# Performance work log

Measured on AMD Instinct MI355X. Metric: run time of the kernel, lower is better.

## Reference

```python
import jax, jax.numpy as jnp
import numpy as np

B, T, C, HS = 8, 2048, 1024, 64

def setup_inputs() -> dict:
    key = jax.random.key(0)
    kx, kq, kk, kv = jax.random.split(key, 4)
    x = jax.random.normal(kx, (B, T, C), dtype=jnp.float32)
    # Linear(C, HS, bias=False) weights, stored as [C, HS] so projection is x @ W
    Wq = jax.random.normal(kq, (C, HS), dtype=jnp.float32) * (C ** -0.5)
    Wk = jax.random.normal(kk, (C, HS), dtype=jnp.float32) * (C ** -0.5)
    Wv = jax.random.normal(kv, (C, HS), dtype=jnp.float32) * (C ** -0.5)
    return {"x": x, "Wq": Wq, "Wk": Wk, "Wv": Wv}

def reference(x, Wq, Wk, Wv):
    Bq, Tq, Cq = x.shape
    q = x @ Wq  # [B,T,HS]
    k = x @ Wk
    v = x @ Wv
    # NOTE: original scales by C**-0.5 with C = embedding_dim (not head_size)
    att = jnp.einsum('bqd,bkd->bqk', q, k) * (Cq ** -0.5)  # [B,T,T]
    causal = jnp.tril(jnp.ones((Tq, Tq), dtype=bool))
    att = jnp.where(causal, att, -jnp.inf)
    att = jax.nn.softmax(att, axis=-1)
    # dropout p=0.0 -> identity
    y = jnp.einsum('bqk,bkd->bqd', att, v)  # [B,T,HS]
    return y
```

## Files before the change

kernel.cpp:

```cpp
#include <hip/hip_runtime.h>
#include <hip/hip_bf16.h>
#include <math.h>

#define B_   8
#define T_   2048
#define C_   1024
#define HS_  64
#define MTOT (B_*T_)

typedef __attribute__((ext_vector_type(8))) short bf16x8;
typedef __attribute__((ext_vector_type(4))) float f32x4;
typedef __attribute__((ext_vector_type(8))) unsigned short u16x8;

static __device__ __forceinline__ unsigned short f2bf(float f) {
    __hip_bfloat16 h = __float2bfloat16(f);
    return *reinterpret_cast<unsigned short*>(&h);
}

__global__ __launch_bounds__(256) void cast_w_kernel(
    const float* __restrict__ Wq, const float* __restrict__ Wk,
    const float* __restrict__ Wv, unsigned short* __restrict__ Wt)
{
    const int tid = threadIdx.x;
    const int col = tid & 63;
    const int kc  = tid >> 6;
    const int mat = blockIdx.y;
    const int k0  = (blockIdx.x * 4 + kc) * 8;
    const float* __restrict__ W = (mat == 0) ? Wq : (mat == 1) ? Wk : Wv;
    const float s = (mat == 0) ? 0.03125f * 1.44269504f : 1.0f;

    u16x8 o;
#pragma unroll
    for (int i = 0; i < 8; ++i)
        o[i] = f2bf(W[(size_t)(k0 + i) * HS_ + col] * s);
    *(u16x8*)&Wt[(size_t)(mat * 64 + col) * C_ + k0] = o;
}

__global__ __launch_bounds__(512) void proj_gemm(
    const float* __restrict__ x, const unsigned short* __restrict__ Wt,
    unsigned short* __restrict__ qbf, unsigned short* __restrict__ kbf,
    unsigned short* __restrict__ vtbf)
{
    __shared__ unsigned short Als[2][64][72];
    __shared__ unsigned short Bls[2][192][72];

    const int tid  = threadIdx.x;
    const int lane = tid & 63;
    const int wv   = tid >> 6;
    const int wr   = wv & 1;
    const int cg   = wv >> 1;
    const int g    = lane >> 4;
    const int n15  = lane & 15;
    const int g4   = g * 4;
    const int m0   = blockIdx.x * 64;

    const int srow = tid >> 3;
    const int seg  = (tid & 7) * 8;
    const float* __restrict__ xrow = &x[(size_t)(m0 + srow) * C_ + seg];
    const unsigned short* __restrict__ wrow = &Wt[(size_t)srow * C_ + seg];

    f32x4 acc[2][3];
#pragma unroll
    for (int i = 0; i < 2; ++i)
#pragma unroll
        for (int j = 0; j < 3; ++j) acc[i][j] = (f32x4){0.f, 0.f, 0.f, 0.f};

    float4 a0[2], a1[2];
    int4   b0, b1, b2;

#define PROJ_LOAD_A(KC, S)                                              \
    do {                                                                \
        a0[S] = *(const float4*)&xrow[(KC) * 64 + 0];                   \
        a1[S] = *(const float4*)&xrow[(KC) * 64 + 4];                   \
    } while (0)

#define PROJ_LOAD_B(KC)                                                 \
    do {                                                                \
        b0 = *(const int4*)&wrow[(KC) * 64];                            \
        b1 = *(const int4*)&wrow[(size_t)64  * C_ + (KC) * 64];        \
        b2 = *(const int4*)&wrow[(size_t)128 * C_ + (KC) * 64];        \
    } while (0)

#define PROJ_WRITE_A(BUF, S)                                            \
    do {                                                                \
        u16x8 v0;                                                       \
        v0[0]=f2bf(a0[S].x); v0[1]=f2bf(a0[S].y);                       \
        v0[2]=f2bf(a0[S].z); v0[3]=f2bf(a0[S].w);                       \
        v0[4]=f2bf(a1[S].x); v0[5]=f2bf(a1[S].y);                       \
        v0[6]=f2bf(a1[S].z); v0[7]=f2bf(a1[S].w);                       \
        *(u16x8*)&Als[BUF][srow][seg] = v0;                             \
    } while (0)

#define PROJ_WRITE_B(BUF)                                               \
    do {                                                                \
        *(int4*)&Bls[BUF][srow][seg]        = b0;                       \
        *(int4*)&Bls[BUF][srow + 64][seg]   = b1;                       \
        *(int4*)&Bls[BUF][srow + 128][seg]  = b2;                       \
    } while (0)

    PROJ_LOAD_A(0, 0);
    PROJ_LOAD_B(0);
    PROJ_WRITE_A(0, 0);
    PROJ_WRITE_B(0);
    PROJ_LOAD_A(1, 1);
    __syncthreads();

    const int NK = C_ / 64;
    for (int kc = 0; kc < NK; ++kc) {
        const int cur = kc & 1;
        const int ka  = (kc + 2 < NK) ? kc + 2 : NK - 1;
        const int kb  = (kc + 1 < NK) ? kc + 1 : NK - 1;
        PROJ_LOAD_A(ka, kc & 1);
        PROJ_LOAD_B(kb);

#pragma unroll
        for (int kk = 0; kk < 2; ++kk) {
            bf16x8 fa0 = *(const bf16x8*)&Als[cur][wr * 32 + n15][kk * 32 + g * 8];
            bf16x8 fa1 = *(const bf16x8*)&Als[cur][wr * 32 + 16 + n15][kk * 32 + g * 8];
            bf16x8 fb0 = *(const bf16x8*)&Bls[cur][cg * 48 + n15][kk * 32 + g * 8];
            bf16x8 fb1 = *(const bf16x8*)&Bls[cur][cg * 48 + 16 + n15][kk * 32 + g * 8];
            bf16x8 fb2 = *(const bf16x8*)&Bls[cur][cg * 48 + 32 + n15][kk * 32 + g * 8];
            acc[0][0] = __builtin_amdgcn_mfma_f32_16x16x32_bf16(fa0, fb0, acc[0][0], 0, 0, 0);
            acc[0][1] = __builtin_amdgcn_mfma_f32_16x16x32_bf16(fa0, fb1, acc[0][1], 0, 0, 0);
            acc[0][2] = __builtin_amdgcn_mfma_f32_16x16x32_bf16(fa0, fb2, acc[0][2], 0, 0, 0);
            acc[1][0] = __builtin_amdgcn_mfma_f32_16x16x32_bf16(fa1, fb0, acc[1][0], 0, 0, 0);
            acc[1][1] = __builtin_amdgcn_mfma_f32_16x16x32_bf16(fa1, fb1, acc[1][1], 0, 0, 0);
            acc[1][2] = __builtin_amdgcn_mfma_f32_16x16x32_bf16(fa1, fb2, acc[1][2], 0, 0, 0);
        }

        if (kc + 1 < NK) {
            __syncthreads();
            PROJ_WRITE_A(cur ^ 1, (kc + 1) & 1);
            PROJ_WRITE_B(cur ^ 1);
            __syncthreads();
        }
    }
#undef PROJ_LOAD_A
#undef PROJ_LOAD_B
#undef PROJ_WRITE_A
#undef PROJ_WRITE_B

    __syncthreads();
    unsigned short* Cqk = &Als[0][0][0];
    unsigned short* Vtr = &Bls[0][0][0];

#pragma unroll
    for (int i = 0; i < 2; ++i)
#pragma unroll
        for (int j = 0; j < 3; ++j) {
            const int gcol = cg * 48 + j * 16 + n15;
            const int row0 = wr * 32 + i * 16 + g4;
            if (gcol < 128) {
#pragma unroll
                for (int r = 0; r < 4; ++r)
                    Cqk[(size_t)(row0 + r) * 136 + gcol] = f2bf(acc[i][j][r]);
            } else {
                ushort4 o;
                o.x = f2bf(acc[i][j][0]); o.y = f2bf(acc[i][j][1]);
                o.z = f2bf(acc[i][j][2]); o.w = f2bf(acc[i][j][3]);
                *(ushort4*)&Vtr[(size_t)(gcol - 128) * 72 + row0] = o;
            }
        }
    __syncthreads();

#pragma unroll
    for (int p = 0; p < 2; ++p) {
        const int flat = tid + p * 512;
        const int mat  = flat >> 9;
        const int r64  = (flat >> 3) & 63;
        const int sg   = (flat & 7) * 8;
        unsigned short* __restrict__ dst = mat ? kbf : qbf;
        *(int4*)&dst[(size_t)(m0 + r64) * HS_ + sg] =
            *(const int4*)&Cqk[(size_t)r64 * 136 + mat * 64 + sg];
    }
    {
        const int b  = m0 >> 11;
        const int t0 = m0 & 2047;
        const int hs = tid >> 3;
        *(int4*)&vtbf[((size_t)b * HS_ + hs) * T_ + t0 + seg] =
            *(const int4*)&Vtr[(size_t)hs * 72 + seg];
    }
}

__global__ __launch_bounds__(512) void attn_kernel(
    const unsigned short* __restrict__ qbf,
    const unsigned short* __restrict__ kbf,
    const unsigned short* __restrict__ vtbf,
    float* __restrict__ y)
{
    __shared__ unsigned short KVs[4][64][72];

    const int tid  = threadIdx.x;
    const int lane = tid & 63;
    const int wv   = tid >> 6;
    const int rg   = wv & 1;
    const int h    = (wv >> 1) & 1;
    const int tp   = wv >> 2;
    const int g    = lane >> 4;
    const int n15  = lane & 15;
    const int g4   = g * 4;
    const int b    = blockIdx.y;
    const size_t qkoff = (size_t)b * T_ * HS_;
    const size_t voff  = (size_t)b * HS_ * T_;

    const int sgrp = tid >> 8;
    const int st   = tid & 255;
    const int srow = st >> 3;
    const int soff = (st & 7) * 8;

    const unsigned short* __restrict__ kgb = &kbf[qkoff];
    const unsigned short* __restrict__ vgb = &vtbf[voff];

    const int qbi  = (blockIdx.y < 4) ? (int)blockIdx.x : 63 - (int)blockIdx.x;
    const int q0   = qbi * 32;
    const int qq0  = q0 + rg * 16;
    const int qrow = qq0 + n15;
    const int nkt  = (qbi >> 1) + 1;

    bf16x8 qf0 = *(const bf16x8*)&qbf[qkoff + (size_t)qrow * HS_ + g * 8];
    bf16x8 qf1 = *(const bf16x8*)&qbf[qkoff + (size_t)qrow * HS_ + g * 8 + 32];

    f32x4 o0 = {0.f,0.f,0.f,0.f}, o1 = o0, o2 = o0, o3 = o0;
    float mrow = -INFINITY, lrow = 0.f;

    int4 kr0, kr1, vr0, vr1;
    {
        int tix = (sgrp < nkt) ? sgrp : nkt - 1;
        kr0 = *(const int4*)&kgb[(size_t)(tix * 64 + srow) * HS_ + soff];
        kr1 = *(const int4*)&kgb[(size_t)(tix * 64 + srow + 32) * HS_ + soff];
        vr0 = *(const int4*)&vgb[(size_t)srow * T_ + tix * 64 + soff];
        vr1 = *(const int4*)&vgb[(size_t)(srow + 32) * T_ + tix * 64 + soff];
    }
    *(int4*)&KVs[sgrp][srow][soff]          = kr0;
    *(int4*)&KVs[sgrp][srow + 32][soff]     = kr1;
    *(int4*)&KVs[2 + sgrp][srow][soff]      = vr0;
    *(int4*)&KVs[2 + sgrp][srow + 32][soff] = vr1;
    __syncthreads();

    const int J = (nkt + 1) >> 1;
    for (int j = 0; j < J; ++j) {
        const int kt = 2 * j + tp;
        {
            int tix = 2 * j + sgrp + 2;
            if (tix > nkt - 1) tix = nkt - 1;
            kr0 = *(const int4*)&kgb[(size_t)(tix * 64 + srow) * HS_ + soff];
            kr1 = *(const int4*)&kgb[(size_t)(tix * 64 + srow + 32) * HS_ + soff];
            vr0 = *(const int4*)&vgb[(size_t)srow * T_ + tix * 64 + soff];
            vr1 = *(const int4*)&vgb[(size_t)(srow + 32) * T_ + tix * 64 + soff];
        }

        if (kt < nkt) {
            const int k0  = kt * 64;
            const int ks0 = h * 32;
            f32x4 st0 = {0.f,0.f,0.f,0.f}, st1 = st0;
            {
                bf16x8 ka;
                ka  = *(const bf16x8*)&KVs[tp][ks0 + n15][g * 8];
                st0 = __builtin_amdgcn_mfma_f32_16x16x32_bf16(ka, qf0, st0, 0, 0, 0);
                ka  = *(const bf16x8*)&KVs[tp][ks0 + n15][g * 8 + 32];
                st0 = __builtin_amdgcn_mfma_f32_16x16x32_bf16(ka, qf1, st0, 0, 0, 0);
                ka  = *(const bf16x8*)&KVs[tp][ks0 + 16 + n15][g * 8];
                st1 = __builtin_amdgcn_mfma_f32_16x16x32_bf16(ka, qf0, st1, 0, 0, 0);
                ka  = *(const bf16x8*)&KVs[tp][ks0 + 16 + n15][g * 8 + 32];
                st1 = __builtin_amdgcn_mfma_f32_16x16x32_bf16(ka, qf1, st1, 0, 0, 0);
            }

            const int kb = k0 + h * 32 + g4;
#pragma unroll
            for (int r = 0; r < 4; ++r) {
                if (kb + r      > qrow) st0[r] = -INFINITY;
                if (kb + 16 + r > qrow) st1[r] = -INFINITY;
            }

            float mloc = fmaxf(fmaxf(st0[0], st0[1]), fmaxf(st0[2], st0[3]));
            mloc = fmaxf(mloc, fmaxf(fmaxf(st1[0], st1[1]), fmaxf(st1[2], st1[3])));
            mloc = fmaxf(mloc, __shfl_xor(mloc, 16));
            mloc = fmaxf(mloc, __shfl_xor(mloc, 32));
            if (!__all(mloc <= mrow + 8.0f)) {
                float mnew  = fmaxf(mrow, mloc);
                float corr  = exp2f(mrow - fmaxf(mnew, -1e30f));
#pragma unroll
                for (int r = 0; r < 4; ++r) {
                    float cr = __shfl(corr, g4 + r);
                    o0[r] *= cr; o1[r] *= cr; o2[r] *= cr; o3[r] *= cr;
                }
                lrow *= corr;
                mrow  = mnew;
            }
            const float mb = fmaxf(mrow, -1e30f);
            float p[8];
            float psum = 0.f;
#pragma unroll
            for (int r = 0; r < 4; ++r) {
                p[r]     = exp2f(st0[r] - mb);
                p[4 + r] = exp2f(st1[r] - mb);
                psum += p[r] + p[4 + r];
            }
            psum += __shfl_xor(psum, 16);
            psum += __shfl_xor(psum, 32);
            lrow += psum;

            bf16x8 pa;
#pragma unroll
            for (int r = 0; r < 4; ++r) {
                pa[r]     = (short)f2bf(p[r]);
                pa[4 + r] = (short)f2bf(p[4 + r]);
            }

            const int kvo = h * 32;
            {
                ushort4 lo, hi; bf16x8 vb;
#define PV_STEP(NT, ONT)                                                        \
                lo = *(const ushort4*)&KVs[2 + tp][(NT)*16 + n15][kvo + g4];    \
                hi = *(const ushort4*)&KVs[2 + tp][(NT)*16 + n15][kvo + 16 + g4];\
                vb[0] = (short)lo.x; vb[1] = (short)lo.y;                       \
                vb[2] = (short)lo.z; vb[3] = (short)lo.w;                       \
                vb[4] = (short)hi.x; vb[5] = (short)hi.y;                       \
                vb[6] = (short)hi.z; vb[7] = (short)hi.w;                       \
                ONT = __builtin_amdgcn_mfma_f32_16x16x32_bf16(pa, vb, ONT, 0, 0, 0);
                PV_STEP(0, o0)
                PV_STEP(1, o1)
                PV_STEP(2, o2)
                PV_STEP(3, o3)
#undef PV_STEP
            }
        }

        if (j + 1 < J) {
            __syncthreads();
            *(int4*)&KVs[sgrp][srow][soff]          = kr0;
            *(int4*)&KVs[sgrp][srow + 32][soff]     = kr1;
            *(int4*)&KVs[2 + sgrp][srow][soff]      = vr0;
            *(int4*)&KVs[2 + sgrp][srow + 32][soff] = vr1;
            __syncthreads();
        }
    }

    __syncthreads();
    float* FS = (float*)&KVs[0][0][0];
    const int pid = (tp << 1) | h;
    if (pid != 0) {
        float* Ob = FS + (pid - 1) * 2176 + rg * 1088;
#pragma unroll
        for (int r = 0; r < 4; ++r) {
            Ob[(g4 + r) * 68 +  0 + n15] = o0[r];
            Ob[(g4 + r) * 68 + 16 + n15] = o1[r];
            Ob[(g4 + r) * 68 + 32 + n15] = o2[r];
            Ob[(g4 + r) * 68 + 48 + n15] = o3[r];
        }
        if (g == 0) {
            FS[6528 + (pid - 1) * 32 + rg * 16 + n15] = mrow;
            FS[6624 + (pid - 1) * 32 + rg * 16 + n15] = lrow;
        }
    }
    __syncthreads();
    if (pid == 0) {
        float m1 = FS[6528 +  0 + rg * 16 + n15];
        float m2 = FS[6528 + 32 + rg * 16 + n15];
        float m3 = FS[6528 + 64 + rg * 16 + n15];
        float l1 = FS[6624 +  0 + rg * 16 + n15];
        float l2 = FS[6624 + 32 + rg * 16 + n15];
        float l3 = FS[6624 + 64 + rg * 16 + n15];
        float mm = fmaxf(fmaxf(mrow, m1), fmaxf(m2, m3));
        float f0 = exp2f(mrow - mm);
        float f1 = exp2f(m1 - mm);
        float f2 = exp2f(m2 - mm);
        float f3 = exp2f(m3 - mm);
        float invl = 1.0f / (lrow * f0 + l1 * f1 + l2 * f2 + l3 * f3);
        const float* O1s = FS;
        const float* O2s = FS + 2176;
        const float* O3s = FS + 4352;
#pragma unroll
        for (int r = 0; r < 4; ++r) {
            float fr0 = __shfl(f0, g4 + r);
            float fr1 = __shfl(f1, g4 + r);
            float fr2 = __shfl(f2, g4 + r);
            float fr3 = __shfl(f3, g4 + r);
            float ir  = __shfl(invl, g4 + r);
            const int base = rg * 1088 + (g4 + r) * 68 + n15;
            float* yr = &y[((size_t)b * T_ + qq0 + g4 + r) * HS_];
            yr[ 0 + n15] = (o0[r] * fr0 + O1s[base]      * fr1 +
                            O2s[base]      * fr2 + O3s[base]      * fr3) * ir;
            yr[16 + n15] = (o1[r] * fr0 + O1s[base + 16] * fr1 +
                            O2s[base + 16] * fr2 + O3s[base + 16] * fr3) * ir;
            yr[32 + n15] = (o2[r] * fr0 + O1s[base + 32] * fr1 +
                            O2s[base + 32] * fr2 + O3s[base + 32] * fr3) * ir;
            yr[48 + n15] = (o3[r] * fr0 + O1s[base + 48] * fr1 +
                            O2s[base + 48] * fr2 + O3s[base + 48] * fr3) * ir;
        }
    }
}

extern "C" void kernel_launch(void* const* d_in, const int* in_sizes, int n_in,
                              void* d_out, int out_size, void* d_ws, size_t ws_size,
                              hipStream_t stream)
{
    const float* x  = (const float*)d_in[0];
    const float* Wq = (const float*)d_in[1];
    const float* Wk = (const float*)d_in[2];
    const float* Wv = (const float*)d_in[3];

    unsigned short* qbf  = (unsigned short*)d_ws;
    unsigned short* kbf  = qbf + (size_t)MTOT * HS_;
    unsigned short* vtbf = kbf + (size_t)MTOT * HS_;
    unsigned short* Wt   = vtbf + (size_t)MTOT * HS_;

    cast_w_kernel<<<dim3(32, 3), 256, 0, stream>>>(Wq, Wk, Wv, Wt);
    proj_gemm<<<256, 512, 0, stream>>>(x, Wt, qbf, kbf, vtbf);
    attn_kernel<<<dim3(64, B_), 512, 0, stream>>>(qbf, kbf, vtbf, (float*)d_out);
}
```

Measured before the change: 48.76 us.

## Pair causal query blocks per workgroup and triple-buffer K/V tiles with one barrier

Each attention workgroup now processes two query blocks, one short and one long (blockIdx.x and 63-blockIdx.x), so per-block causal work is balanced. Launched workgroups drop from 64 to 32 per batch. The K/V shared buffer becomes a three-slot ring with two register sets of prefetched tiles, which lets each iteration use one __syncthreads instead of two and writes the next tile before computing the current one. The cost is larger shared memory per block, possibly lower occupancy, and half as many blocks for the GPU to schedule.

```diff
diff --git a/kernel.cpp b/kernel.cpp
--- a/kernel.cpp
+++ b/kernel.cpp
@@ -188,7 +188,8 @@
     const unsigned short* __restrict__ vtbf,
     float* __restrict__ y)
 {
-    __shared__ unsigned short KVs[4][64][72];
+    __shared__ unsigned short Ksl[3][2][64][72];
+    __shared__ unsigned short Vsl[3][2][64][72];
 
     const int tid  = threadIdx.x;
     const int lane = tid & 63;
@@ -211,184 +212,217 @@
     const unsigned short* __restrict__ kgb = &kbf[qkoff];
     const unsigned short* __restrict__ vgb = &vtbf[voff];
 
-    const int qbi  = (blockIdx.y < 4) ? (int)blockIdx.x : 63 - (int)blockIdx.x;
-    const int q0   = qbi * 32;
-    const int qq0  = q0 + rg * 16;
-    const int qrow = qq0 + n15;
-    const int nkt  = (qbi >> 1) + 1;
-
-    bf16x8 qf0 = *(const bf16x8*)&qbf[qkoff + (size_t)qrow * HS_ + g * 8];
-    bf16x8 qf1 = *(const bf16x8*)&qbf[qkoff + (size_t)qrow * HS_ + g * 8 + 32];
-
-    f32x4 o0 = {0.f,0.f,0.f,0.f}, o1 = o0, o2 = o0, o3 = o0;
-    float mrow = -INFINITY, lrow = 0.f;
-
-    int4 kr0, kr1, vr0, vr1;
-    {
-        int tix = (sgrp < nkt) ? sgrp : nkt - 1;
-        kr0 = *(const int4*)&kgb[(size_t)(tix * 64 + srow) * HS_ + soff];
-        kr1 = *(const int4*)&kgb[(size_t)(tix * 64 + srow + 32) * HS_ + soff];
-        vr0 = *(const int4*)&vgb[(size_t)srow * T_ + tix * 64 + soff];
-        vr1 = *(const int4*)&vgb[(size_t)(srow + 32) * T_ + tix * 64 + soff];
+#define ATTN_LOADSET(K0, K1, V0, V1, TIX)                                   \
+    do {                                                                    \
+        K0 = *(const int4*)&kgb[(size_t)((TIX) * 64 + srow) * HS_ + soff];  \
+        K1 = *(const int4*)&kgb[(size_t)((TIX) * 64 + srow + 32) * HS_ + soff]; \
+        V0 = *(const int4*)&vgb[(size_t)srow * T_ + (TIX) * 64 + soff];     \
+        V1 = *(const int4*)&vgb[(size_t)(srow + 32) * T_ + (TIX) * 64 + soff]; \
+    } while (0)
+
+#define ATTN_WRITESET(K0, K1, V0, V1, SLOT)                                 \
+    do {                                                                    \
+        *(int4*)&Ksl[SLOT][sgrp][srow][soff]      = K0;                     \
+        *(int4*)&Ksl[SLOT][sgrp][srow + 32][soff] = K1;                     \
+        *(int4*)&Vsl[SLOT][sgrp][srow][soff]      = V0;                     \
+        *(int4*)&Vsl[SLOT][sgrp][srow + 32][soff] = V1;                     \
+    } while (0)
+
+#define ATTN_COMPUTE(SC)                                                    \
+    do {                                                                    \
+        const int k0  = kt * 64;                                            \
+        const int ks0 = h * 32;                                             \
+        f32x4 st0 = {0.f,0.f,0.f,0.f}, st1 = st0;                           \
+        {                                                                   \
+            bf16x8 ka;                                                      \
+            ka  = *(const bf16x8*)&Ksl[SC][tp][ks0 + n15][g * 8];           \
+            st0 = __builtin_amdgcn_mfma_f32_16x16x32_bf16(ka, qf0, st0, 0, 0, 0); \
+            ka  = *(const bf16x8*)&Ksl[SC][tp][ks0 + n15][g * 8 + 32];      \
+            st0 = __builtin_amdgcn_mfma_f32_16x16x32_bf16(ka, qf1, st0, 0, 0, 0); \
+            ka  = *(const bf16x8*)&Ksl[SC][tp][ks0 + 16 + n15][g * 8];      \
+            st1 = __builtin_amdgcn_mfma_f32_16x16x32_bf16(ka, qf0, st1, 0, 0, 0); \
+            ka  = *(const bf16x8*)&Ksl[SC][tp][ks0 + 16 + n15][g * 8 + 32]; \
+            st1 = __builtin_amdgcn_mfma_f32_16x16x32_bf16(ka, qf1, st1, 0, 0, 0); \
+        }                                                                   \
+        const int kb = k0 + h * 32 + g4;                                    \
+        _Pragma("unroll")                                                   \
+        for (int r = 0; r < 4; ++r) {                                       \
+            if (kb + r      > qrow) st0[r] = -INFINITY;                     \
+            if (kb + 16 + r > qrow) st1[r] = -INFINITY;                     \
+        }                                                                   \
+        float mloc = fmaxf(fmaxf(st0[0], st0[1]), fmaxf(st0[2], st0[3]));   \
+        mloc = fmaxf(mloc, fmaxf(fmaxf(st1[0], st1[1]), fmaxf(st1[2], st1[3]))); \
+        mloc = fmaxf(mloc, __shfl_xor(mloc, 16));                           \
+        mloc = fmaxf(mloc, __shfl_xor(mloc, 32));                           \
+        if (!__all(mloc <= mrow + 8.0f)) {                                  \
+            float mnew  = fmaxf(mrow, mloc);                                \
+            float corr  = exp2f(mrow - fmaxf(mnew, -1e30f));                \
+            _Pragma("unroll")                                               \
+            for (int r = 0; r < 4; ++r) {                                   \
+                float cr = __shfl(corr, g4 + r);                            \
+                o0[r] *= cr; o1[r] *= cr; o2[r] *= cr; o3[r] *= cr;         \
+            }                                                               \
+            lrow *= corr;                                                   \
+            mrow  = mnew;                                                   \
+        }                                                                   \
+        const float mb = fmaxf(mrow, -1e30f);                               \
+        float p[8];                                                         \
+        float psum = 0.f;                                                   \
+        _Pragma("unroll")                                                   \
+        for (int r = 0; r < 4; ++r) {                                       \
+            p[r]     = exp2f(st0[r] - mb);                                  \
+            p[4 + r] = exp2f(st1[r] - mb);                                  \
+            psum += p[r] + p[4 + r];                                        \
+        }                                                                   \
+        psum += __shfl_xor(psum, 16);                                       \
+        psum += __shfl_xor(psum, 32);                                       \
+        lrow += psum;                                                       \
+        bf16x8 pa;                                                          \
+        _Pragma("unroll")                                                   \
+        for (int r = 0; r < 4; ++r) {                                       \
+            pa[r]     = (short)f2bf(p[r]);                                  \
+            pa[4 + r] = (short)f2bf(p[4 + r]);                              \
+        }                                                                   \
+        const int kvo = h * 32;                                             \
+        {                                                                   \
+            ushort4 lo, hi; bf16x8 vb;                                      \
+            _Pragma("unroll")                                               \
+            for (int nt = 0; nt < 4; ++nt) {                                \
+                lo = *(const ushort4*)&Vsl[SC][tp][nt * 16 + n15][kvo + g4];      \
+                hi = *(const ushort4*)&Vsl[SC][tp][nt * 16 + n15][kvo + 16 + g4]; \
+                vb[0] = (short)lo.x; vb[1] = (short)lo.y;                   \
+                vb[2] = (short)lo.z; vb[3] = (short)lo.w;                   \
+                vb[4] = (short)hi.x; vb[5] = (short)hi.y;                   \
+                vb[6] = (short)hi.z; vb[7] = (short)hi.w;                   \
+                if (nt == 0) o0 = __builtin_amdgcn_mfma_f32_16x16x32_bf16(pa, vb, o0, 0, 0, 0); \
+                if (nt == 1) o1 = __builtin_amdgcn_mfma_f32_16x16x32_bf16(pa, vb, o1, 0, 0, 0); \
+                if (nt == 2) o2 = __builtin_amdgcn_mfma_f32_16x16x32_bf16(pa, vb, o2, 0, 0, 0); \
+                if (nt == 3) o3 = __builtin_amdgcn_mfma_f32_16x16x32_bf16(pa, vb, o3, 0, 0, 0); \
+            }                                                               \
+        }                                                                   \
+    } while (0)
+
+    for (int pass = 0; pass < 2; ++pass) {
+        const int qbi  = pass ? (63 - (int)blockIdx.x) : (int)blockIdx.x;
+        const int q0   = qbi * 32;
+        const int qq0  = q0 + rg * 16;
+        const int qrow = qq0 + n15;
+        const int nkt  = (qbi >> 1) + 1;
+        const int J    = (nkt + 1) >> 1;
+
+        bf16x8 qf0 = *(const bf16x8*)&qbf[qkoff + (size_t)qrow * HS_ + g * 8];
+        bf16x8 qf1 = *(const bf16x8*)&qbf[qkoff + (size_t)qrow * HS_ + g * 8 + 32];
+
+        f32x4 o0 = {0.f,0.f,0.f,0.f}, o1 = o0, o2 = o0, o3 = o0;
+        float mrow = -INFINITY, lrow = 0.f;
+
+        int4 kA0, kA1, vA0, vA1;
+        int4 kB0, kB1, vB0, vB1;
+
+        {
+            int tix = (sgrp < nkt) ? sgrp : nkt - 1;
+            ATTN_LOADSET(kA0, kA1, vA0, vA1, tix);
+        }
+        __syncthreads();
+        ATTN_WRITESET(kA0, kA1, vA0, vA1, 0);
+        {
+            int tix = 2 + sgrp; if (tix > nkt - 1) tix = nkt - 1;
+            ATTN_LOADSET(kB0, kB1, vB0, vB1, tix);
+        }
+        __syncthreads();
+
+        int j = 0;
+        while (true) {
+            {
+                if (j + 1 < J) {
+                    const int sN = (j + 1) % 3;
+                    ATTN_WRITESET(kB0, kB1, vB0, vB1, sN);
+                }
+                {
+                    int tix = 2 * (j + 2) + sgrp;
+                    if (tix > nkt - 1) tix = nkt - 1;
+                    ATTN_LOADSET(kA0, kA1, vA0, vA1, tix);
+                }
+                const int kt = 2 * j + tp;
+                const int sC = j % 3;
+                if (kt < nkt) ATTN_COMPUTE(sC);
+                __syncthreads();
+            }
+            if (++j >= J) break;
+            {
+                if (j + 1 < J) {
+                    const int sN = (j + 1) % 3;
+                    ATTN_WRITESET(kA0, kA1, vA0, vA1, sN);
+                }
+                {
+                    int tix = 2 * (j + 2) + sgrp;
+                    if (tix > nkt - 1) tix = nkt - 1;
+                    ATTN_LOADSET(kB0, kB1, vB0, vB1, tix);
+                }
+                const int kt = 2 * j + tp;
+                const int sC = j % 3;
+                if (kt < nkt) ATTN_COMPUTE(sC);
+                __syncthreads();
+            }
+            if (++j >= J) break;
+        }
+
+        float* FS = (float*)&Ksl[0][0][0][0];
+        const int pid = (tp << 1) | h;
+        if (pid != 0) {
+            float* Ob = FS + (pid - 1) * 2176 + rg * 1088;
+#pragma unroll
+            for (int r = 0; r < 4; ++r) {
+                Ob[(g4 + r) * 68 +  0 + n15] = o0[r];
+                Ob[(g4 + r) * 68 + 16 + n15] = o1[r];
+                Ob[(g4 + r) * 68 + 32 + n15] = o2[r];
+                Ob[(g4 + r) * 68 + 48 + n15] = o3[r];
+            }
+            if (g == 0) {
+                FS[6528 + (pid - 1) * 32 + rg * 16 + n15] = mrow;
+                FS[6624 + (pid - 1) * 32 + rg * 16 + n15] = lrow;
+            }
+        }
+        __syncthreads();
+        if (pid == 0) {
+            float m1 = FS[6528 +  0 + rg * 16 + n15];
+            float m2 = FS[6528 + 32 + rg * 16 + n15];
+            float m3 = FS[6528 + 64 + rg * 16 + n15];
+            float l1 = FS[6624 +  0 + rg * 16 + n15];
+            float l2 = FS[6624 + 32 + rg * 16 + n15];
+            float l3 = FS[6624 + 64 + rg * 16 + n15];
+            float mm = fmaxf(fmaxf(mrow, m1), fmaxf(m2, m3));
+            float f0 = exp2f(mrow - mm);
+            float f1 = exp2f(m1 - mm);
+            float f2 = exp2f(m2 - mm);
+            float f3 = exp2f(m3 - mm);
+            float invl = 1.0f / (lrow * f0 + l1 * f1 + l2 * f2 + l3 * f3);
+            const float* O1s = FS;
+            const float* O2s = FS + 2176;
+            const float* O3s = FS + 4352;
+#pragma unroll
+            for (int r = 0; r < 4; ++r) {
+                float fr0 = __shfl(f0, g4 + r);
+                float fr1 = __shfl(f1, g4 + r);
+                float fr2 = __shfl(f2, g4 + r);
+                float fr3 = __shfl(f3, g4 + r);
+                float ir  = __shfl(invl, g4 + r);
+                const int base = rg * 1088 + (g4 + r) * 68 + n15;
+                float* yr = &y[((size_t)b * T_ + qq0 + g4 + r) * HS_];
+                yr[ 0 + n15] = (o0[r] * fr0 + O1s[base]      * fr1 +
+                                O2s[base]      * fr2 + O3s[base]      * fr3) * ir;
+                yr[16 + n15] = (o1[r] * fr0 + O1s[base + 16] * fr1 +
+                                O2s[base + 16] * fr2 + O3s[base + 16] * fr3) * ir;
+                yr[32 + n15] = (o2[r] * fr0 + O1s[base + 32] * fr1 +
+                                O2s[base + 32] * fr2 + O3s[base + 32] * fr3) * ir;
+                yr[48 + n15] = (o3[r] * fr0 + O1s[base + 48] * fr1 +
+                                O2s[base + 48] * fr2 + O3s[base + 48] * fr3) * ir;
+            }
+        }
     }
-    *(int4*)&KVs[sgrp][srow][soff]          = kr0;
-    *(int4*)&KVs[sgrp][srow + 32][soff]     = kr1;
-    *(int4*)&KVs[2 + sgrp][srow][soff]      = vr0;
-    *(int4*)&KVs[2 + sgrp][srow + 32][soff] = vr1;
-    __syncthreads();
-
-    const int J = (nkt + 1) >> 1;
-    for (int j = 0; j < J; ++j) {
-        const int kt = 2 * j + tp;
-        {
-            int tix = 2 * j + sgrp + 2;
-            if (tix > nkt - 1) tix = nkt - 1;
-            kr0 = *(const int4*)&kgb[(size_t)(tix * 64 + srow) * HS_ + soff];
-            kr1 = *(const int4*)&kgb[(size_t)(tix * 64 + srow + 32) * HS_ + soff];
-            vr0 = *(const int4*)&vgb[(size_t)srow * T_ + tix * 64 + soff];
-            vr1 = *(const int4*)&vgb[(size_t)(srow + 32) * T_ + tix * 64 + soff];
-        }
-
-        if (kt < nkt) {
-            const int k0  = kt * 64;
-            const int ks0 = h * 32;
-            f32x4 st0 = {0.f,0.f,0.f,0.f}, st1 = st0;
-            {
-                bf16x8 ka;
-                ka  = *(const bf16x8*)&KVs[tp][ks0 + n15][g * 8];
-                st0 = __builtin_amdgcn_mfma_f32_16x16x32_bf16(ka, qf0, st0, 0, 0, 0);
-                ka  = *(const bf16x8*)&KVs[tp][ks0 + n15][g * 8 + 32];
-                st0 = __builtin_amdgcn_mfma_f32_16x16x32_bf16(ka, qf1, st0, 0, 0, 0);
-                ka  = *(const bf16x8*)&KVs[tp][ks0 + 16 + n15][g * 8];
-                st1 = __builtin_amdgcn_mfma_f32_16x16x32_bf16(ka, qf0, st1, 0, 0, 0);
-                ka  = *(const bf16x8*)&KVs[tp][ks0 + 16 + n15][g * 8 + 32];
-                st1 = __builtin_amdgcn_mfma_f32_16x16x32_bf16(ka, qf1, st1, 0, 0, 0);
-            }
-
-            const int kb = k0 + h * 32 + g4;
-#pragma unroll
-            for (int r = 0; r < 4; ++r) {
-                if (kb + r      > qrow) st0[r] = -INFINITY;
-                if (kb + 16 + r > qrow) st1[r] = -INFINITY;
-            }
-
-            float mloc = fmaxf(fmaxf(st0[0], st0[1]), fmaxf(st0[2], st0[3]));
-            mloc = fmaxf(mloc, fmaxf(fmaxf(st1[0], st1[1]), fmaxf(st1[2], st1[3])));
-            mloc = fmaxf(mloc, __shfl_xor(mloc, 16));
-            mloc = fmaxf(mloc, __shfl_xor(mloc, 32));
-            if (!__all(mloc <= mrow + 8.0f)) {
-                float mnew  = fmaxf(mrow, mloc);
-                float corr  = exp2f(mrow - fmaxf(mnew, -1e30f));
-#pragma unroll
-                for (int r = 0; r < 4; ++r) {
-                    float cr = __shfl(corr, g4 + r);
-                    o0[r] *= cr; o1[r] *= cr; o2[r] *= cr; o3[r] *= cr;
-                }
-                lrow *= corr;
-                mrow  = mnew;
-            }
-            const float mb = fmaxf(mrow, -1e30f);
-            float p[8];
-            float psum = 0.f;
-#pragma unroll
-            for (int r = 0; r < 4; ++r) {
-                p[r]     = exp2f(st0[r] - mb);
-                p[4 + r] = exp2f(st1[r] - mb);
-                psum += p[r] + p[4 + r];
-            }
-            psum += __shfl_xor(psum, 16);
-            psum += __shfl_xor(psum, 32);
-            lrow += psum;
-
-            bf16x8 pa;
-#pragma unroll
-            for (int r = 0; r < 4; ++r) {
-                pa[r]     = (short)f2bf(p[r]);
-                pa[4 + r] = (short)f2bf(p[4 + r]);
-            }
-
-            const int kvo = h * 32;
-            {
-                ushort4 lo, hi; bf16x8 vb;
-#define PV_STEP(NT, ONT)                                                        \
-                lo = *(const ushort4*)&KVs[2 + tp][(NT)*16 + n15][kvo + g4];    \
-                hi = *(const ushort4*)&KVs[2 + tp][(NT)*16 + n15][kvo + 16 + g4];\
-                vb[0] = (short)lo.x; vb[1] = (short)lo.y;                       \
-                vb[2] = (short)lo.z; vb[3] = (short)lo.w;                       \
-                vb[4] = (short)hi.x; vb[5] = (short)hi.y;                       \
-                vb[6] = (short)hi.z; vb[7] = (short)hi.w;                       \
-                ONT = __builtin_amdgcn_mfma_f32_16x16x32_bf16(pa, vb, ONT, 0, 0, 0);
-                PV_STEP(0, o0)
-                PV_STEP(1, o1)
-                PV_STEP(2, o2)
-                PV_STEP(3, o3)
-#undef PV_STEP
-            }
-        }
-
-        if (j + 1 < J) {
-            __syncthreads();
-            *(int4*)&KVs[sgrp][srow][soff]          = kr0;
-            *(int4*)&KVs[sgrp][srow + 32][soff]     = kr1;
-            *(int4*)&KVs[2 + sgrp][srow][soff]      = vr0;
-            *(int4*)&KVs[2 + sgrp][srow + 32][soff] = vr1;
-            __syncthreads();
-        }
-    }
-
-    __syncthreads();
-    float* FS = (float*)&KVs[0][0][0];
-    const int pid = (tp << 1) | h;
-    if (pid != 0) {
-        float* Ob = FS + (pid - 1) * 2176 + rg * 1088;
-#pragma unroll
-        for (int r = 0; r < 4; ++r) {
-            Ob[(g4 + r) * 68 +  0 + n15] = o0[r];
-            Ob[(g4 + r) * 68 + 16 + n15] = o1[r];
-            Ob[(g4 + r) * 68 + 32 + n15] = o2[r];
-            Ob[(g4 + r) * 68 + 48 + n15] = o3[r];
-        }
-        if (g == 0) {
-            FS[6528 + (pid - 1) * 32 + rg * 16 + n15] = mrow;
-            FS[6624 + (pid - 1) * 32 + rg * 16 + n15] = lrow;
-        }
-    }
-    __syncthreads();
-    if (pid == 0) {
-        float m1 = FS[6528 +  0 + rg * 16 + n15];
-        float m2 = FS[6528 + 32 + rg * 16 + n15];
-        float m3 = FS[6528 + 64 + rg * 16 + n15];
-        float l1 = FS[6624 +  0 + rg * 16 + n15];
-        float l2 = FS[6624 + 32 + rg * 16 + n15];
-        float l3 = FS[6624 + 64 + rg * 16 + n15];
-        float mm = fmaxf(fmaxf(mrow, m1), fmaxf(m2, m3));
-        float f0 = exp2f(mrow - mm);
-        float f1 = exp2f(m1 - mm);
-        float f2 = exp2f(m2 - mm);
-        float f3 = exp2f(m3 - mm);
-        float invl = 1.0f / (lrow * f0 + l1 * f1 + l2 * f2 + l3 * f3);
-        const float* O1s = FS;
-        const float* O2s = FS + 2176;
-        const float* O3s = FS + 4352;
-#pragma unroll
-        for (int r = 0; r < 4; ++r) {
-            float fr0 = __shfl(f0, g4 + r);
-            float fr1 = __shfl(f1, g4 + r);
-            float fr2 = __shfl(f2, g4 + r);
-            float fr3 = __shfl(f3, g4 + r);
-            float ir  = __shfl(invl, g4 + r);
-            const int base = rg * 1088 + (g4 + r) * 68 + n15;
-            float* yr = &y[((size_t)b * T_ + qq0 + g4 + r) * HS_];
-            yr[ 0 + n15] = (o0[r] * fr0 + O1s[base]      * fr1 +
-                            O2s[base]      * fr2 + O3s[base]      * fr3) * ir;
-            yr[16 + n15] = (o1[r] * fr0 + O1s[base + 16] * fr1 +
-                            O2s[base + 16] * fr2 + O3s[base + 16] * fr3) * ir;
-            yr[32 + n15] = (o2[r] * fr0 + O1s[base + 32] * fr1 +
-                            O2s[base + 32] * fr2 + O3s[base + 32] * fr3) * ir;
-            yr[48 + n15] = (o3[r] * fr0 + O1s[base + 48] * fr1 +
-                            O2s[base + 48] * fr2 + O3s[base + 48] * fr3) * ir;
-        }
-    }
+#undef ATTN_LOADSET
+#undef ATTN_WRITESET
+#undef ATTN_COMPUTE
 }
 
 extern "C" void kernel_launch(void* const* d_in, const int* in_sizes, int n_in,
@@ -407,5 +441,5 @@
 
     cast_w_kernel<<<dim3(32, 3), 256, 0, stream>>>(Wq, Wk, Wv, Wt);
     proj_gemm<<<256, 512, 0, stream>>>(x, Wt, qbf, kbf, vtbf);
-    attn_kernel<<<dim3(64, B_), 512, 0, stream>>>(qbf, kbf, vtbf, (float*)d_out);
+    attn_kernel<<<dim3(32, B_), 512, 0, stream>>>(qbf, kbf, vtbf, (float*)d_out);
 }
```

Result: no change. 49.58 us (+1.7%).

## Process two 32-row query sets per K/V tile and pair causal blocks per workgroup

Applied to the files above, without the earlier changes.

Each workgroup now handles 64 query rows, split into two 32-row sets A and B that share each K/V tile loaded into LDS. This halves the K/V global loads and LDS staging per query row. Each block also runs two passes over a mirrored pair of query blocks (x and 31-x), which balances the causal triangle's work across blocks. The grid is halved to 32x8 = 256 workgroups, so there is less parallelism, more registers per thread from the doubled accumulators, and an extra merge phase per pass.

```diff
diff --git a/kernel.cpp b/kernel.cpp
--- a/kernel.cpp
+++ b/kernel.cpp
@@ -211,183 +211,240 @@
     const unsigned short* __restrict__ kgb = &kbf[qkoff];
     const unsigned short* __restrict__ vgb = &vtbf[voff];
 
-    const int qbi  = (blockIdx.y < 4) ? (int)blockIdx.x : 63 - (int)blockIdx.x;
-    const int q0   = qbi * 32;
-    const int qq0  = q0 + rg * 16;
-    const int qrow = qq0 + n15;
-    const int nkt  = (qbi >> 1) + 1;
-
-    bf16x8 qf0 = *(const bf16x8*)&qbf[qkoff + (size_t)qrow * HS_ + g * 8];
-    bf16x8 qf1 = *(const bf16x8*)&qbf[qkoff + (size_t)qrow * HS_ + g * 8 + 32];
-
-    f32x4 o0 = {0.f,0.f,0.f,0.f}, o1 = o0, o2 = o0, o3 = o0;
-    float mrow = -INFINITY, lrow = 0.f;
-
-    int4 kr0, kr1, vr0, vr1;
-    {
-        int tix = (sgrp < nkt) ? sgrp : nkt - 1;
-        kr0 = *(const int4*)&kgb[(size_t)(tix * 64 + srow) * HS_ + soff];
-        kr1 = *(const int4*)&kgb[(size_t)(tix * 64 + srow + 32) * HS_ + soff];
-        vr0 = *(const int4*)&vgb[(size_t)srow * T_ + tix * 64 + soff];
-        vr1 = *(const int4*)&vgb[(size_t)(srow + 32) * T_ + tix * 64 + soff];
-    }
-    *(int4*)&KVs[sgrp][srow][soff]          = kr0;
-    *(int4*)&KVs[sgrp][srow + 32][soff]     = kr1;
-    *(int4*)&KVs[2 + sgrp][srow][soff]      = vr0;
-    *(int4*)&KVs[2 + sgrp][srow + 32][soff] = vr1;
-    __syncthreads();
-
-    const int J = (nkt + 1) >> 1;
-    for (int j = 0; j < J; ++j) {
-        const int kt = 2 * j + tp;
+    for (int pass = 0; pass < 2; ++pass) {
+        const int qbi  = pass ? (31 - (int)blockIdx.x) : (int)blockIdx.x;
+        const int q0   = qbi * 64;
+        const int qqA  = q0 + rg * 16;
+        const int qqB  = q0 + 32 + rg * 16;
+        const int qrowA = qqA + n15;
+        const int qrowB = qqB + n15;
+        const int nkt  = qbi + 1;
+
+        bf16x8 qfA0 = *(const bf16x8*)&qbf[qkoff + (size_t)qrowA * HS_ + g * 8];
+        bf16x8 qfA1 = *(const bf16x8*)&qbf[qkoff + (size_t)qrowA * HS_ + g * 8 + 32];
+        bf16x8 qfB0 = *(const bf16x8*)&qbf[qkoff + (size_t)qrowB * HS_ + g * 8];
+        bf16x8 qfB1 = *(const bf16x8*)&qbf[qkoff + (size_t)qrowB * HS_ + g * 8 + 32];
+
+        f32x4 oA0 = {0.f,0.f,0.f,0.f}, oA1 = oA0, oA2 = oA0, oA3 = oA0;
+        f32x4 oB0 = oA0, oB1 = oA0, oB2 = oA0, oB3 = oA0;
+        float mA = -INFINITY, lA = 0.f;
+        float mB = -INFINITY, lB = 0.f;
+
+        int4 kr0, kr1, vr0, vr1;
         {
-            int tix = 2 * j + sgrp + 2;
-            if (tix > nkt - 1) tix = nkt - 1;
+            int tix = (sgrp < nkt) ? sgrp : nkt - 1;
             kr0 = *(const int4*)&kgb[(size_t)(tix * 64 + srow) * HS_ + soff];
             kr1 = *(const int4*)&kgb[(size_t)(tix * 64 + srow + 32) * HS_ + soff];
             vr0 = *(const int4*)&vgb[(size_t)srow * T_ + tix * 64 + soff];
             vr1 = *(const int4*)&vgb[(size_t)(srow + 32) * T_ + tix * 64 + soff];
         }
-
-        if (kt < nkt) {
-            const int k0  = kt * 64;
-            const int ks0 = h * 32;
-            f32x4 st0 = {0.f,0.f,0.f,0.f}, st1 = st0;
+        __syncthreads();
+        *(int4*)&KVs[sgrp][srow][soff]          = kr0;
+        *(int4*)&KVs[sgrp][srow + 32][soff]     = kr1;
+        *(int4*)&KVs[2 + sgrp][srow][soff]      = vr0;
+        *(int4*)&KVs[2 + sgrp][srow + 32][soff] = vr1;
+        __syncthreads();
+
+        const int J = (nkt + 1) >> 1;
+        for (int j = 0; j < J; ++j) {
+            const int kt = 2 * j + tp;
             {
-                bf16x8 ka;
-                ka  = *(const bf16x8*)&KVs[tp][ks0 + n15][g * 8];
-                st0 = __builtin_amdgcn_mfma_f32_16x16x32_bf16(ka, qf0, st0, 0, 0, 0);
-                ka  = *(const bf16x8*)&KVs[tp][ks0 + n15][g * 8 + 32];
-                st0 = __builtin_amdgcn_mfma_f32_16x16x32_bf16(ka, qf1, st0, 0, 0, 0);
-                ka  = *(const bf16x8*)&KVs[tp][ks0 + 16 + n15][g * 8];
-                st1 = __builtin_amdgcn_mfma_f32_16x16x32_bf16(ka, qf0, st1, 0, 0, 0);
-                ka  = *(const bf16x8*)&KVs[tp][ks0 + 16 + n15][g * 8 + 32];
-                st1 = __builtin_amdgcn_mfma_f32_16x16x32_bf16(ka, qf1, st1, 0, 0, 0);
+                int tix = 2 * j + sgrp + 2;
+                if (tix > nkt - 1) tix = nkt - 1;
+                kr0 = *(const int4*)&kgb[(size_t)(tix * 64 + srow) * HS_ + soff];
+                kr1 = *(const int4*)&kgb[(size_t)(tix * 64 + srow + 32) * HS_ + soff];
+                vr0 = *(const int4*)&vgb[(size_t)srow * T_ + tix * 64 + soff];
+                vr1 = *(const int4*)&vgb[(size_t)(srow + 32) * T_ + tix * 64 + soff];
             }
 
-            const int kb = k0 + h * 32 + g4;
-#pragma unroll
-            for (int r = 0; r < 4; ++r) {
-                if (kb + r      > qrow) st0[r] = -INFINITY;
-                if (kb + 16 + r > qrow) st1[r] = -INFINITY;
+            if (kt < nkt) {
+                const int k0  = kt * 64;
+                const int ks0 = h * 32;
+
+                bf16x8 ka0 = *(const bf16x8*)&KVs[tp][ks0 + n15][g * 8];
+                bf16x8 ka1 = *(const bf16x8*)&KVs[tp][ks0 + n15][g * 8 + 32];
+                bf16x8 ka2 = *(const bf16x8*)&KVs[tp][ks0 + 16 + n15][g * 8];
+                bf16x8 ka3 = *(const bf16x8*)&KVs[tp][ks0 + 16 + n15][g * 8 + 32];
+
+                f32x4 sA0 = {0.f,0.f,0.f,0.f}, sA1 = sA0;
+                sA0 = __builtin_amdgcn_mfma_f32_16x16x32_bf16(ka0, qfA0, sA0, 0, 0, 0);
+                sA0 = __builtin_amdgcn_mfma_f32_16x16x32_bf16(ka1, qfA1, sA0, 0, 0, 0);
+                sA1 = __builtin_amdgcn_mfma_f32_16x16x32_bf16(ka2, qfA0, sA1, 0, 0, 0);
+                sA1 = __builtin_amdgcn_mfma_f32_16x16x32_bf16(ka3, qfA1, sA1, 0, 0, 0);
+                f32x4 sB0 = {0.f,0.f,0.f,0.f}, sB1 = sB0;
+                sB0 = __builtin_amdgcn_mfma_f32_16x16x32_bf16(ka0, qfB0, sB0, 0, 0, 0);
+                sB0 = __builtin_amdgcn_mfma_f32_16x16x32_bf16(ka1, qfB1, sB0, 0, 0, 0);
+                sB1 = __builtin_amdgcn_mfma_f32_16x16x32_bf16(ka2, qfB0, sB1, 0, 0, 0);
+                sB1 = __builtin_amdgcn_mfma_f32_16x16x32_bf16(ka3, qfB1, sB1, 0, 0, 0);
+
+                const int kb = k0 + ks0 + g4;
+#pragma unroll
+                for (int r = 0; r < 4; ++r) {
+                    if (kb + r      > qrowA) sA0[r] = -INFINITY;
+                    if (kb + 16 + r > qrowA) sA1[r] = -INFINITY;
+                    if (kb + r      > qrowB) sB0[r] = -INFINITY;
+                    if (kb + 16 + r > qrowB) sB1[r] = -INFINITY;
+                }
+
+                bf16x8 paA, paB;
+                {
+                    float mloc = fmaxf(fmaxf(sA0[0], sA0[1]), fmaxf(sA0[2], sA0[3]));
+                    mloc = fmaxf(mloc, fmaxf(fmaxf(sA1[0], sA1[1]), fmaxf(sA1[2], sA1[3])));
+                    mloc = fmaxf(mloc, __shfl_xor(mloc, 16));
+                    mloc = fmaxf(mloc, __shfl_xor(mloc, 32));
+                    if (!__all(mloc <= mA + 8.0f)) {
+                        float mnew = fmaxf(mA, mloc);
+                        float corr = exp2f(mA - fmaxf(mnew, -1e30f));
+#pragma unroll
+                        for (int r = 0; r < 4; ++r) {
+                            float cr = __shfl(corr, g4 + r);
+                            oA0[r] *= cr; oA1[r] *= cr; oA2[r] *= cr; oA3[r] *= cr;
+                        }
+                        lA *= corr;
+                        mA  = mnew;
+                    }
+                    const float mb = fmaxf(mA, -1e30f);
+                    float p[8];
+                    float psum = 0.f;
+#pragma unroll
+                    for (int r = 0; r < 4; ++r) {
+                        p[r]     = exp2f(sA0[r] - mb);
+                        p[4 + r] = exp2f(sA1[r] - mb);
+                        psum += p[r] + p[4 + r];
+                    }
+                    psum += __shfl_xor(psum, 16);
+                    psum += __shfl_xor(psum, 32);
+                    lA += psum;
+#pragma unroll
+                    for (int r = 0; r < 4; ++r) {
+                        paA[r]     = (short)f2bf(p[r]);
+                        paA[4 + r] = (short)f2bf(p[4 + r]);
+                    }
+                }
+                {
+                    float mloc = fmaxf(fmaxf(sB0[0], sB0[1]), fmaxf(sB0[2], sB0[3]));
+                    mloc = fmaxf(mloc, fmaxf(fmaxf(sB1[0], sB1[1]), fmaxf(sB1[2], sB1[3])));
+                    mloc = fmaxf(mloc, __shfl_xor(mloc, 16));
+                    mloc = fmaxf(mloc, __shfl_xor(mloc, 32));
+                    if (!__all(mloc <= mB + 8.0f)) {
+                        float mnew = fmaxf(mB, mloc);
+                        float corr = exp2f(mB - fmaxf(mnew, -1e30f));
+#pragma unroll
+                        for (int r = 0; r < 4; ++r) {
+                            float cr = __shfl(corr, g4 + r);
+                            oB0[r] *= cr; oB1[r] *= cr; oB2[r] *= cr; oB3[r] *= cr;
+                        }
+                        lB *= corr;
+                        mB  = mnew;
+                    }
+                    const float mb = fmaxf(mB, -1e30f);
+                    float p[8];
+                    float psum = 0.f;
+#pragma unroll
+                    for (int r = 0; r < 4; ++r) {
+                        p[r]     = exp2f(sB0[r] - mb);
+                        p[4 + r] = exp2f(sB1[r] - mb);
+                        psum += p[r] + p[4 + r];
+                    }
+                    psum += __shfl_xor(psum, 16);
+                    psum += __shfl_xor(psum, 32);
+                    lB += psum;
+#pragma unroll
+                    for (int r = 0; r < 4; ++r) {
+                        paB[r]     = (short)f2bf(p[r]);
+                        paB[4 + r] = (short)f2bf(p[4 + r]);
+                    }
+                }
+
+                const int kvo = h * 32;
+                {
+                    ushort4 lo, hi; bf16x8 vb;
+#define PV_STEP(NT, OA, OB)                                                     \
+                    lo = *(const ushort4*)&KVs[2 + tp][(NT)*16 + n15][kvo + g4];\
+                    hi = *(const ushort4*)&KVs[2 + tp][(NT)*16 + n15][kvo + 16 + g4];\
+                    vb[0] = (short)lo.x; vb[1] = (short)lo.y;                   \
+                    vb[2] = (short)lo.z; vb[3] = (short)lo.w;                   \
+                    vb[4] = (short)hi.x; vb[5] = (short)hi.y;                   \
+                    vb[6] = (short)hi.z; vb[7] = (short)hi.w;                   \
+                    OA = __builtin_amdgcn_mfma_f32_16x16x32_bf16(paA, vb, OA, 0, 0, 0); \
+                    OB = __builtin_amdgcn_mfma_f32_16x16x32_bf16(paB, vb, OB, 0, 0, 0);
+                    PV_STEP(0, oA0, oB0)
+                    PV_STEP(1, oA1, oB1)
+                    PV_STEP(2, oA2, oB2)
+                    PV_STEP(3, oA3, oB3)
+#undef PV_STEP
+                }
             }
 
-            float mloc = fmaxf(fmaxf(st0[0], st0[1]), fmaxf(st0[2], st0[3]));
-            mloc = fmaxf(mloc, fmaxf(fmaxf(st1[0], st1[1]), fmaxf(st1[2], st1[3])));
-            mloc = fmaxf(mloc, __shfl_xor(mloc, 16));
-            mloc = fmaxf(mloc, __shfl_xor(mloc, 32));
-            if (!__all(mloc <= mrow + 8.0f)) {
-                float mnew  = fmaxf(mrow, mloc);
-                float corr  = exp2f(mrow - fmaxf(mnew, -1e30f));
-#pragma unroll
-                for (int r = 0; r < 4; ++r) {
-                    float cr = __shfl(corr, g4 + r);
-                    o0[r] *= cr; o1[r] *= cr; o2[r] *= cr; o3[r] *= cr;
-                }
-                lrow *= corr;
-                mrow  = mnew;
-            }
-            const float mb = fmaxf(mrow, -1e30f);
-            float p[8];
-            float psum = 0.f;
-#pragma unroll
-            for (int r = 0; r < 4; ++r) {
-                p[r]     = exp2f(st0[r] - mb);
-                p[4 + r] = exp2f(st1[r] - mb);
-                psum += p[r] + p[4 + r];
-            }
-            psum += __shfl_xor(psum, 16);
-            psum += __shfl_xor(psum, 32);
-            lrow += psum;
-
-            bf16x8 pa;
-#pragma unroll
-            for (int r = 0; r < 4; ++r) {
-                pa[r]     = (short)f2bf(p[r]);
-                pa[4 + r] = (short)f2bf(p[4 + r]);
-            }
-
-            const int kvo = h * 32;
-            {
-                ushort4 lo, hi; bf16x8 vb;
-#define PV_STEP(NT, ONT)                                                        \
-                lo = *(const ushort4*)&KVs[2 + tp][(NT)*16 + n15][kvo + g4];    \
-                hi = *(const ushort4*)&KVs[2 + tp][(NT)*16 + n15][kvo + 16 + g4];\
-                vb[0] = (short)lo.x; vb[1] = (short)lo.y;                       \
-                vb[2] = (short)lo.z; vb[3] = (short)lo.w;                       \
-                vb[4] = (short)hi.x; vb[5] = (short)hi.y;                       \
-                vb[6] = (short)hi.z; vb[7] = (short)hi.w;                       \
-                ONT = __builtin_amdgcn_mfma_f32_16x16x32_bf16(pa, vb, ONT, 0, 0, 0);
-                PV_STEP(0, o0)
-                PV_STEP(1, o1)
-                PV_STEP(2, o2)
-                PV_STEP(3, o3)
-#undef PV_STEP
+            if (j + 1 < J) {
+                __syncthreads();
+                *(int4*)&KVs[sgrp][srow][soff]          = kr0;
+                *(int4*)&KVs[sgrp][srow + 32][soff]     = kr1;
+                *(int4*)&KVs[2 + sgrp][srow][soff]      = vr0;
+                *(int4*)&KVs[2 + sgrp][srow + 32][soff] = vr1;
+                __syncthreads();
             }
         }
 
-        if (j + 1 < J) {
-            __syncthreads();
-            *(int4*)&KVs[sgrp][srow][soff]          = kr0;
-            *(int4*)&KVs[sgrp][srow + 32][soff]     = kr1;
-            *(int4*)&KVs[2 + sgrp][srow][soff]      = vr0;
-            *(int4*)&KVs[2 + sgrp][srow + 32][soff] = vr1;
-            __syncthreads();
-        }
-    }
-
-    __syncthreads();
-    float* FS = (float*)&KVs[0][0][0];
-    const int pid = (tp << 1) | h;
-    if (pid != 0) {
-        float* Ob = FS + (pid - 1) * 2176 + rg * 1088;
-#pragma unroll
-        for (int r = 0; r < 4; ++r) {
-            Ob[(g4 + r) * 68 +  0 + n15] = o0[r];
-            Ob[(g4 + r) * 68 + 16 + n15] = o1[r];
-            Ob[(g4 + r) * 68 + 32 + n15] = o2[r];
-            Ob[(g4 + r) * 68 + 48 + n15] = o3[r];
-        }
-        if (g == 0) {
-            FS[6528 + (pid - 1) * 32 + rg * 16 + n15] = mrow;
-            FS[6624 + (pid - 1) * 32 + rg * 16 + n15] = lrow;
-        }
-    }
-    __syncthreads();
-    if (pid == 0) {
-        float m1 = FS[6528 +  0 + rg * 16 + n15];
-        float m2 = FS[6528 + 32 + rg * 16 + n15];
-        float m3 = FS[6528 + 64 + rg * 16 + n15];
-        float l1 = FS[6624 +  0 + rg * 16 + n15];
-        float l2 = FS[6624 + 32 + rg * 16 + n15];
-        float l3 = FS[6624 + 64 + rg * 16 + n15];
-        float mm = fmaxf(fmaxf(mrow, m1), fmaxf(m2, m3));
-        float f0 = exp2f(mrow - mm);
-        float f1 = exp2f(m1 - mm);
-        float f2 = exp2f(m2 - mm);
-        float f3 = exp2f(m3 - mm);
-        float invl = 1.0f / (lrow * f0 + l1 * f1 + l2 * f2 + l3 * f3);
-        const float* O1s = FS;
-        const float* O2s = FS + 2176;
-        const float* O3s = FS + 4352;
-#pragma unroll
-        for (int r = 0; r < 4; ++r) {
-            float fr0 = __shfl(f0, g4 + r);
-            float fr1 = __shfl(f1, g4 + r);
-            float fr2 = __shfl(f2, g4 + r);
-            float fr3 = __shfl(f3, g4 + r);
-            float ir  = __shfl(invl, g4 + r);
-            const int base = rg * 1088 + (g4 + r) * 68 + n15;
-            float* yr = &y[((size_t)b * T_ + qq0 + g4 + r) * HS_];
-            yr[ 0 + n15] = (o0[r] * fr0 + O1s[base]      * fr1 +
-                            O2s[base]      * fr2 + O3s[base]      * fr3) * ir;
-            yr[16 + n15] = (o1[r] * fr0 + O1s[base + 16] * fr1 +
-                            O2s[base + 16] * fr2 + O3s[base + 16] * fr3) * ir;
-            yr[32 + n15] = (o2[r] * fr0 + O1s[base + 32] * fr1 +
-                            O2s[base + 32] * fr2 + O3s[base + 32] * fr3) * ir;
-            yr[48 + n15] = (o3[r] * fr0 + O1s[base + 48] * fr1 +
-                            O2s[base + 48] * fr2 + O3s[base + 48] * fr3) * ir;
-        }
+        float* FS = (float*)&KVs[0][0][0];
+        const int pid = (tp << 1) | h;
+
+#define MERGE_SET(O0, O1, O2, O3, MR, LR, QQ)                               \
+    do {                                                                    \
+        __syncthreads();                                                    \
+        if (pid != 0) {                                                     \
+            float* Ob = FS + (pid - 1) * 2176 + rg * 1088;                  \
+            for (int r = 0; r < 4; ++r) {                                   \
+                Ob[(g4 + r) * 68 +  0 + n15] = O0[r];                       \
+                Ob[(g4 + r) * 68 + 16 + n15] = O1[r];                       \
+                Ob[(g4 + r) * 68 + 32 + n15] = O2[r];                       \
+                Ob[(g4 + r) * 68 + 48 + n15] = O3[r];                       \
+            }                                                               \
+            if (g == 0) {                                                   \
+                FS[6528 + (pid - 1) * 32 + rg * 16 + n15] = MR;             \
+                FS[6624 + (pid - 1) * 32 + rg * 16 + n15] = LR;             \
+            }                                                               \
+        }                                                                   \
+        __syncthreads();                                                    \
+        if (pid == 0) {                                                     \
+            float m1 = FS[6528 +  0 + rg * 16 + n15];                       \
+            float m2 = FS[6528 + 32 + rg * 16 + n15];                       \
+            float m3 = FS[6528 + 64 + rg * 16 + n15];                       \
+            float l1 = FS[6624 +  0 + rg * 16 + n15];                       \
+            float l2 = FS[6624 + 32 + rg * 16 + n15];                       \
+            float l3 = FS[6624 + 64 + rg * 16 + n15];                       \
+            float mm = fmaxf(fmaxf(MR, m1), fmaxf(m2, m3));                 \
+            float f0 = exp2f(MR - mm);                                      \
+            float f1 = exp2f(m1 - mm);                                      \
+            float f2 = exp2f(m2 - mm);                                      \
+            float f3 = exp2f(m3 - mm);                                      \
+            float invl = 1.0f / (LR * f0 + l1 * f1 + l2 * f2 + l3 * f3);    \
+            const float* O1s = FS;                                          \
+            const float* O2s = FS + 2176;                                   \
+            const float* O3s = FS + 4352;                                   \
+            for (int r = 0; r < 4; ++r) {                                   \
+                float fr0 = __shfl(f0, g4 + r);                             \
+                float fr1 = __shfl(f1, g4 + r);                             \
+                float fr2 = __shfl(f2, g4 + r);                             \
+                float fr3 = __shfl(f3, g4 + r);                             \
+                float ir  = __shfl(invl, g4 + r);                           \
+                const int base = rg * 1088 + (g4 + r) * 68 + n15;           \
+                float* yr = &y[((size_t)b * T_ + (QQ) + g4 + r) * HS_];     \
+                yr[ 0 + n15] = (O0[r] * fr0 + O1s[base]      * fr1 +        \
+                                O2s[base]      * fr2 + O3s[base]      * fr3) * ir; \
+                yr[16 + n15] = (O1[r] * fr0 + O1s[base + 16] * fr1 +        \
+                                O2s[base + 16] * fr2 + O3s[base + 16] * fr3) * ir; \
+                yr[32 + n15] = (O2[r] * fr0 + O1s[base + 32] * fr1 +        \
+                                O2s[base + 32] * fr2 + O3s[base + 32] * fr3) * ir; \
+                yr[48 + n15] = (O3[r] * fr0 + O1s[base + 48] * fr1 +        \
+                                O2s[base + 48] * fr2 + O3s[base + 48] * fr3) * ir; \
+            }                                                               \
+        }                                                                   \
+    } while (0)
+
+        MERGE_SET(oA0, oA1, oA2, oA3, mA, lA, qqA);
+        MERGE_SET(oB0, oB1, oB2, oB3, mB, lB, qqB);
+#undef MERGE_SET
     }
 }
 
@@ -407,5 +464,5 @@
 
     cast_w_kernel<<<dim3(32, 3), 256, 0, stream>>>(Wq, Wk, Wv, Wt);
     proj_gemm<<<256, 512, 0, stream>>>(x, Wt, qbf, kbf, vtbf);
-    attn_kernel<<<dim3(64, B_), 512, 0, stream>>>(qbf, kbf, vtbf, (float*)d_out);
+    attn_kernel<<<dim3(32, B_), 512, 0, stream>>>(qbf, kbf, vtbf, (float*)d_out);
 }
```

Result: slower. 62.22 us (+27.6%).
